# Kernel optimization log

Measured on AMD Instinct MI355X. Metric: run time of the kernel, lower is better.

The kernel has to match this reference:

```python
import jax, jax.numpy as jnp
import numpy as np

EMBED_DIM = 768
HEADS = 8
HEAD_DIM = 128  # gnn_hidden_dim
OUT_DIM = HEADS * HEAD_DIM  # 1024, concat=True
NEG_SLOPE = 0.2  # PyG GATConv leaky_relu slope


def setup_inputs() -> dict:
    key = jax.random.key(0)
    ks = jax.random.split(key, 12)
    N, E = 10000, 160000
    x = jax.random.normal(ks[0], (N, EMBED_DIM), dtype=jnp.float32)
    edge_index = jax.random.randint(ks[1], (2, E), 0, N, dtype=jnp.int32)
    edge_attr = jax.random.uniform(ks[2], (E, 1), dtype=jnp.float32)
    # GATConv params (single layer, edge_dim=1)
    sc = 1.0 / np.sqrt(EMBED_DIM)
    W = jax.random.normal(ks[3], (EMBED_DIM, OUT_DIM), dtype=jnp.float32) * sc
    att_src = jax.random.normal(ks[4], (HEADS, HEAD_DIM), dtype=jnp.float32) * 0.1
    att_dst = jax.random.normal(ks[5], (HEADS, HEAD_DIM), dtype=jnp.float32) * 0.1
    W_edge = jax.random.normal(ks[6], (1, OUT_DIM), dtype=jnp.float32)
    att_edge = jax.random.normal(ks[7], (HEADS, HEAD_DIM), dtype=jnp.float32) * 0.1
    bias = jnp.zeros((OUT_DIM,), dtype=jnp.float32)
    # final classifier: in = 3*OUT_DIM (global pool + text node + image node)
    clf_W = jax.random.normal(ks[8], (3 * OUT_DIM, 2), dtype=jnp.float32) * (1.0 / np.sqrt(3 * OUT_DIM))
    clf_b = jnp.zeros((2,), dtype=jnp.float32)
    return {
        'x': x, 'edge_index': edge_index, 'edge_attr': edge_attr,
        'text_idx': 0, 'image_idx': 1,
        'W': W, 'att_src': att_src, 'att_dst': att_dst,
        'W_edge': W_edge, 'att_edge': att_edge, 'bias': bias,
        'clf_W': clf_W, 'clf_b': clf_b,
    }


def gat_layer(x, edge_index, edge_attr, W, att_src, att_dst, W_edge, att_edge, bias):
    N = x.shape[0]
    # add self-loops with edge_attr = mean of existing edge_attr (PyG default fill_value='mean')
    loop = jnp.arange(N, dtype=edge_index.dtype)
    ei = jnp.concatenate([edge_index, jnp.stack([loop, loop])], axis=1)
    ea_mean = jnp.mean(edge_attr, axis=0, keepdims=True)
    ea = jnp.concatenate([edge_attr, jnp.broadcast_to(ea_mean, (N, edge_attr.shape[1]))], axis=0)
    src, dst = ei[0], ei[1]
    xs = (x @ W).reshape(N, HEADS, HEAD_DIM)             # [N, H, C]
    a_src = jnp.einsum('nhc,hc->nh', xs, att_src)        # per-node src logits
    a_dst = jnp.einsum('nhc,hc->nh', xs, att_dst)
    e_emb = (ea @ W_edge).reshape(-1, HEADS, HEAD_DIM)   # [Etot, H, C]
    a_edge = jnp.einsum('ehc,hc->eh', e_emb, att_edge)
    alpha = jax.nn.leaky_relu(a_src[src] + a_dst[dst] + a_edge, NEG_SLOPE)  # [Etot, H]
    # softmax over incoming edges of each dst node
    m = jax.ops.segment_max(alpha, dst, num_segments=N)
    ex = jnp.exp(alpha - m[dst])
    denom = jax.ops.segment_sum(ex, dst, num_segments=N)
    w = ex / denom[dst]                                  # normalized attention [Etot, H]
    msg = xs[src] * w[:, :, None]                        # [Etot, H, C]
    out = jax.ops.segment_sum(msg, dst, num_segments=N)  # [N, H, C]
    return out.reshape(N, OUT_DIM) + bias


def reference(x, edge_index, edge_attr, text_idx, image_idx,
              W, att_src, att_dst, W_edge, att_edge, bias, clf_W, clf_b):
    # single GAT layer (num_gat_layers=1 -> no ELU/dropout after, eval mode)
    h = gat_layer(x, edge_index, edge_attr, W, att_src, att_dst, W_edge, att_edge, bias)
    g = jnp.mean(h, axis=0, keepdims=True)               # global_mean_pool, batch=None
    t = h[text_idx][None, :]
    im = h[image_idx][None, :]
    fused = jnp.concatenate([g, t, im], axis=1)          # [1, 3*OUT_DIM]
    logits = fused @ clf_W + clf_b                       # [1, 2]
    return logits
```

## Files before the change

kernel.cpp:

```cpp
#include <hip/hip_runtime.h>

#define NN 10000
#define EE 160000
#define ETOT (EE + NN)
#define EMB 768
#define ODIM 1024
#define NEG 0.2f
#define CAP 56

#define OFF_P      0
#define OFF_Q      12288
#define OFF_EAACC  12296
#define OFF_CNTD   12304
#define OFF_CNTS   22304
#define ZERO_START 12296
#define ZERO_CNT   20008
#define OFF_A      32304
#define OFF_SRCD   192304
#define OFF_AED    752304
#define OFF_DSTS   1312304
#define OFF_AES    1872304
#define OFF_RDEN   2432304
#define OFF_Z      2512304
#define OFF_YPART  2524592

#define SELF_MARK 3.0e38f

__global__ __launch_bounds__(256) void k1f(
    const float* __restrict__ W, const float* __restrict__ att_src,
    const float* __restrict__ att_dst, const float* __restrict__ W_edge,
    const float* __restrict__ att_edge, const float* __restrict__ edge_attr,
    const float* __restrict__ bias, const float* __restrict__ clf_W,
    const float* __restrict__ clf_b, float* __restrict__ out,
    const int* __restrict__ ei, float* __restrict__ ws) {
  int b = blockIdx.x;
  if (b < 48) {
    int tid = b * 256 + threadIdx.x;
    int k = tid >> 4, j = tid & 15, h = j & 7;
    const float* att = (j < 8) ? att_src : att_dst;
    const float4* wp = (const float4*)(W + k * ODIM + h * 128);
    const float4* ap = (const float4*)(att + h * 128);
    float acc = 0.f;
    #pragma unroll 8
    for (int c = 0; c < 32; ++c) {
      float4 w4 = wp[c], a4 = ap[c];
      acc += w4.x * a4.x + w4.y * a4.y + w4.z * a4.z + w4.w * a4.w;
    }
    ws[OFF_P + k * 16 + j] = acc;
  } else if (b == 48) {
    if (threadIdx.x < 8) {
      int h = threadIdx.x;
      float acc = 0.f;
      #pragma unroll 8
      for (int c = 0; c < 128; ++c) acc += W_edge[h * 128 + c] * att_edge[h * 128 + c];
      ws[OFF_Q + h] = acc;
    }
  } else if (b == 49) {
    __shared__ float red[8];
    int t = threadIdx.x;
    float b0 = 0.f, b1 = 0.f;
    for (int i = t; i < 3072; i += 256) {
      float f = bias[i & 1023];
      b0 += f * clf_W[2 * i];
      b1 += f * clf_W[2 * i + 1];
    }
    #pragma unroll
    for (int o = 32; o > 0; o >>= 1) {
      b0 += __shfl_down(b0, o, 64);
      b1 += __shfl_down(b1, o, 64);
    }
    if ((t & 63) == 0) { red[(t >> 6) * 2] = b0; red[(t >> 6) * 2 + 1] = b1; }
    __syncthreads();
    if (t == 0) {
      out[0] = clf_b[0] + red[0] + red[2] + red[4] + red[6];
      out[1] = clf_b[1] + red[1] + red[3] + red[5] + red[7];
    }
  } else if (b < 114) {
    int bi = b - 50;
    float acc = 0.f;
    for (int i = bi * 256 + threadIdx.x; i < EE; i += 64 * 256) acc += edge_attr[i];
    #pragma unroll
    for (int off = 32; off > 0; off >>= 1) acc += __shfl_down(acc, off, 64);
    if ((threadIdx.x & 63) == 0) atomicAdd(&ws[OFF_EAACC], acc);
  } else {
    int e = (b - 114) * 256 + threadIdx.x;
    if (e >= ETOT) return;
    int src, dst; float ea;
    if (e < EE) { src = ei[e]; dst = ei[EE + e]; ea = edge_attr[e]; }
    else { src = dst = e - EE; ea = SELF_MARK; }
    int* cntd = (int*)(ws + OFF_CNTD);
    int* cnts = (int*)(ws + OFF_CNTS);
    int pd = atomicAdd(&cntd[dst], 1);
    if (pd < CAP) {
      ((int*)(ws + OFF_SRCD))[dst * CAP + pd] = src;
      ws[OFF_AED + dst * CAP + pd] = ea;
    }
    int ps = atomicAdd(&cnts[src], 1);
    if (ps < CAP) {
      ((int*)(ws + OFF_DSTS))[src * CAP + ps] = dst;
      ws[OFF_AES + src * CAP + ps] = ea;
    }
  }
}

__global__ __launch_bounds__(256) void kAx(const float* __restrict__ x,
                                           float* __restrict__ ws) {
  __shared__ float smem[12288];
  for (int i = threadIdx.x; i < 3072; i += 256)
    ((float4*)smem)[i] = ((const float4*)(ws + OFF_P))[i];
  __syncthreads();
  int nl = threadIdx.x & 31, cg = threadIdx.x >> 5;
  int n = blockIdx.x * 32 + nl;
  float a[16];
  #pragma unroll
  for (int j = 0; j < 16; ++j) a[j] = 0.f;
  if (n < NN) {
    const float4* xr = (const float4*)(x + n * EMB + cg * 96);
    for (int kk = 0; kk < 24; ++kk) {
      float4 xv = xr[kk];
      const float* pr = &smem[(cg * 96 + kk * 4) * 16];
      #pragma unroll
      for (int j = 0; j < 16; ++j) a[j] += xv.x * pr[j];
      #pragma unroll
      for (int j = 0; j < 16; ++j) a[j] += xv.y * pr[16 + j];
      #pragma unroll
      for (int j = 0; j < 16; ++j) a[j] += xv.z * pr[32 + j];
      #pragma unroll
      for (int j = 0; j < 16; ++j) a[j] += xv.w * pr[48 + j];
    }
  }
  __syncthreads();
  #pragma unroll
  for (int j = 0; j < 16; ++j) smem[(cg * 16 + j) * 33 + nl] = a[j];
  __syncthreads();
  for (int w = threadIdx.x; w < 512; w += 256) {
    int rnl = w >> 4, j = w & 15;
    int nn = blockIdx.x * 32 + rnl;
    if (nn < NN) {
      float s = 0.f;
      #pragma unroll
      for (int c2 = 0; c2 < 8; ++c2) s += smem[(c2 * 16 + j) * 33 + rnl];
      ws[OFF_A + nn * 16 + j] = s;
    }
  }
}

__global__ __launch_bounds__(128) void kD(float* __restrict__ ws) {
  int t = blockIdx.x * 128 + threadIdx.x;
  int dst = t >> 3, h = t & 7;
  int deg = ((const int*)(ws + OFF_CNTD))[dst];
  if (deg > CAP) deg = CAP;
  float adh = ws[OFF_A + dst * 16 + 8 + h];
  float qh = ws[OFF_Q + h];
  float mean = ws[OFF_EAACC] * (1.0f / EE);
  const int* srow = (const int*)(ws + OFF_SRCD) + dst * CAP;
  const float* aerow = ws + OFF_AED + dst * CAP;
  float den = 0.f;
  for (int j = 0; j < deg; ++j) {
    float ae = aerow[j];
    if (ae > 1e37f) ae = mean;
    float v = ws[OFF_A + srow[j] * 16 + h] + adh + ae * qh;
    v = (v >= 0.f) ? v : NEG * v;
    den += __expf(v);
  }
  ws[OFF_RDEN + t] = 1.0f / den;
}

__global__ __launch_bounds__(256) void kSYZ(const float* __restrict__ x,
                                            const int* __restrict__ tptr,
                                            const int* __restrict__ iptr,
                                            float* __restrict__ ws) {
  __shared__ float sL[512];
  __shared__ int srcS[CAP];
  float mean = ws[OFF_EAACC] * (1.0f / EE);
  if (blockIdx.x < 471) {
    int bx = blockIdx.x / 3, c = blockIdx.x % 3;
    int base = bx * 64;
    for (int t = threadIdx.x; t < 512; t += 256) {
      int n = base + (t >> 3), h = t & 7;
      float s = 0.f;
      if (n < NN) {
        int deg = ((const int*)(ws + OFF_CNTS))[n];
        if (deg > CAP) deg = CAP;
        float ash = ws[OFF_A + n * 16 + h];
        float qh = ws[OFF_Q + h];
        const int* drow = (const int*)(ws + OFF_DSTS) + n * CAP;
        const float* aerow = ws + OFF_AES + n * CAP;
        for (int j = 0; j < deg; ++j) {
          int dd = drow[j];
          float ae = aerow[j];
          if (ae > 1e37f) ae = mean;
          float v = ash + ws[OFF_A + dd * 16 + 8 + h] + ae * qh;
          v = (v >= 0.f) ? v : NEG * v;
          s += __expf(v) * ws[OFF_RDEN + dd * 8 + h];
        }
      }
      sL[t] = s;
    }
    __syncthreads();
    int col = c * 256 + threadIdx.x;
    float acc[8];
    #pragma unroll
    for (int h = 0; h < 8; ++h) acc[h] = 0.f;
    int nmax = (NN - base < 64) ? (NN - base) : 64;
    for (int i = 0; i < nmax; ++i) {
      float xv = x[(base + i) * EMB + col];
      const float* sv = &sL[i * 8];
      #pragma unroll
      for (int h = 0; h < 8; ++h) acc[h] += xv * sv[h];
    }
    float* yp = ws + OFF_YPART + bx * 6144 + col;
    #pragma unroll
    for (int h = 0; h < 8; ++h) yp[h * 768] = acc[h];
  } else {
    int r = blockIdx.x - 471;
    int d = r / 3, kc = r % 3;
    int target = (d == 0) ? tptr[0] : iptr[0];
    int deg = ((const int*)(ws + OFF_CNTD))[target];
    if (deg > CAP) deg = CAP;
    for (int idx = threadIdx.x; idx < deg * 8; idx += 256) {
      int j = idx >> 3, h = idx & 7;
      int srcj = ((const int*)(ws + OFF_SRCD))[target * CAP + j];
      float ae = ws[OFF_AED + target * CAP + j];
      if (ae > 1e37f) ae = mean;
      float v = ws[OFF_A + srcj * 16 + h] + ws[OFF_A + target * 16 + 8 + h]
              + ae * ws[OFF_Q + h];
      v = (v >= 0.f) ? v : NEG * v;
      sL[idx] = __expf(v) * ws[OFF_RDEN + target * 8 + h];
      if (h == 0) srcS[j] = srcj;
    }
    __syncthreads();
    int col = kc * 256 + threadIdx.x;
    float acc[8];
    #pragma unroll
    for (int h = 0; h < 8; ++h) acc[h] = 0.f;
    for (int j = 0; j < deg; ++j) {
      float xv = x[srcS[j] * EMB + col];
      const float* wv = &sL[j * 8];
      #pragma unroll
      for (int h = 0; h < 8; ++h) acc[h] += wv[h] * xv;
    }
    #pragma unroll
    for (int h = 0; h < 8; ++h) ws[OFF_Z + (d * 8 + h) * EMB + col] = acc[h];
  }
}

__global__ __launch_bounds__(128) void k8(const float* __restrict__ W,
                                          const float* __restrict__ clf_W,
                                          float* __restrict__ out,
                                          float* __restrict__ ws) {
  __shared__ float vL[144];
  __shared__ float red[4];
  int h = blockIdx.x, kc = blockIdx.y, kbase = kc * 48;
  for (int i = threadIdx.x; i < 144; i += 128) {
    int d = i / 48, k = i - d * 48;
    float v;
    if (d == 0) {
      float acc = 0.f;
      for (int b = 0; b < 157; ++b)
        acc += ws[OFF_YPART + b * 6144 + h * 768 + kbase + k];
      v = acc * (1.0f / NN);
    } else {
      v = ws[OFF_Z + ((d - 1) * 8 + h) * 768 + kbase + k];
    }
    vL[i] = v;
  }
  __syncthreads();
  int c = threadIdx.x;
  float a0 = 0.f, a1 = 0.f, a2 = 0.f;
  #pragma unroll 4
  for (int k = 0; k < 48; ++k) {
    float wv = W[(kbase + k) * ODIM + h * 128 + c];
    a0 += vL[k] * wv;
    a1 += vL[48 + k] * wv;
    a2 += vL[96 + k] * wv;
  }
  int ib = h * 128 + c;
  float l0 = a0 * clf_W[2 * ib] + a1 * clf_W[2 * (1024 + ib)]
           + a2 * clf_W[2 * (2048 + ib)];
  float l1 = a0 * clf_W[2 * ib + 1] + a1 * clf_W[2 * (1024 + ib) + 1]
           + a2 * clf_W[2 * (2048 + ib) + 1];
  #pragma unroll
  for (int o = 32; o > 0; o >>= 1) {
    l0 += __shfl_down(l0, o, 64);
    l1 += __shfl_down(l1, o, 64);
  }
  if ((threadIdx.x & 63) == 0) {
    red[(threadIdx.x >> 6) * 2] = l0;
    red[(threadIdx.x >> 6) * 2 + 1] = l1;
  }
  __syncthreads();
  if (threadIdx.x == 0) {
    atomicAdd(&out[0], red[0] + red[2]);
    atomicAdd(&out[1], red[1] + red[3]);
  }
}

extern "C" void kernel_launch(void* const* d_in, const int* in_sizes, int n_in,
                              void* d_out, int out_size, void* d_ws, size_t ws_size,
                              hipStream_t stream) {
  const float* x        = (const float*)d_in[0];
  const int*   ei       = (const int*)d_in[1];
  const float* edge_attr= (const float*)d_in[2];
  const int*   tptr     = (const int*)d_in[3];
  const int*   iptr     = (const int*)d_in[4];
  const float* W        = (const float*)d_in[5];
  const float* att_src  = (const float*)d_in[6];
  const float* att_dst  = (const float*)d_in[7];
  const float* W_edge   = (const float*)d_in[8];
  const float* att_edge = (const float*)d_in[9];
  const float* bias     = (const float*)d_in[10];
  const float* clf_W    = (const float*)d_in[11];
  const float* clf_b    = (const float*)d_in[12];
  float* ws  = (float*)d_ws;
  float* out = (float*)d_out;

  hipMemsetAsync(ws + ZERO_START, 0, ZERO_CNT * sizeof(float), stream);
  k1f<<<779, 256, 0, stream>>>(W, att_src, att_dst, W_edge, att_edge, edge_attr,
                               bias, clf_W, clf_b, out, ei, ws);
  kAx<<<313, 256, 0, stream>>>(x, ws);
  kD<<<625, 128, 0, stream>>>(ws);
  kSYZ<<<477, 256, 0, stream>>>(x, tptr, iptr, ws);
  dim3 g8(8, 16);
  k8<<<g8, 128, 0, stream>>>(W, clf_W, out, ws);
}
```

Measured before the change: 192.8 us.

## Merge memset and five kernels into one cooperative persistent kernel with grid syncs

```diff
diff --git a/kernel.cpp b/kernel.cpp
--- a/kernel.cpp
+++ b/kernel.cpp
@@ -1,4 +1,7 @@
 #include <hip/hip_runtime.h>
+#include <hip/hip_cooperative_groups.h>
+
+namespace cg = cooperative_groups;
 
 #define NN 10000
 #define EE 160000
@@ -25,17 +28,26 @@
 #define OFF_YPART  2524592
 
 #define SELF_MARK 3.0e38f
-
-__global__ __launch_bounds__(256) void k1f(
-    const float* __restrict__ W, const float* __restrict__ att_src,
-    const float* __restrict__ att_dst, const float* __restrict__ W_edge,
-    const float* __restrict__ att_edge, const float* __restrict__ edge_attr,
+#define GRID 512
+#define GSZ (GRID * 256)
+
+__global__ __launch_bounds__(256, 2) void mega(
+    const float* __restrict__ x, const int* __restrict__ ei,
+    const float* __restrict__ edge_attr, const int* __restrict__ tptr,
+    const int* __restrict__ iptr, const float* __restrict__ W,
+    const float* __restrict__ att_src, const float* __restrict__ att_dst,
+    const float* __restrict__ W_edge, const float* __restrict__ att_edge,
     const float* __restrict__ bias, const float* __restrict__ clf_W,
     const float* __restrict__ clf_b, float* __restrict__ out,
-    const int* __restrict__ ei, float* __restrict__ ws) {
-  int b = blockIdx.x;
-  if (b < 48) {
-    int tid = b * 256 + threadIdx.x;
+    float* __restrict__ ws) {
+  cg::grid_group grid = cg::this_grid();
+  __shared__ float smem[12288];
+  const int gtid = blockIdx.x * 256 + threadIdx.x;
+
+  for (int i = gtid; i < ZERO_CNT; i += GSZ) ws[ZERO_START + i] = 0.f;
+  grid.sync();
+
+  for (int tid = gtid; tid < 12288; tid += GSZ) {
     int k = tid >> 4, j = tid & 15, h = j & 7;
     const float* att = (j < 8) ? att_src : att_dst;
     const float4* wp = (const float4*)(W + k * ODIM + h * 128);
@@ -46,17 +58,17 @@
       float4 w4 = wp[c], a4 = ap[c];
       acc += w4.x * a4.x + w4.y * a4.y + w4.z * a4.z + w4.w * a4.w;
     }
-    ws[OFF_P + k * 16 + j] = acc;
-  } else if (b == 48) {
-    if (threadIdx.x < 8) {
-      int h = threadIdx.x;
-      float acc = 0.f;
-      #pragma unroll 8
-      for (int c = 0; c < 128; ++c) acc += W_edge[h * 128 + c] * att_edge[h * 128 + c];
-      ws[OFF_Q + h] = acc;
-    }
-  } else if (b == 49) {
-    __shared__ float red[8];
+    ws[OFF_P + tid] = acc;
+  }
+  if (gtid < 8) {
+    int h = gtid;
+    float acc = 0.f;
+    #pragma unroll 8
+    for (int c = 0; c < 128; ++c) acc += W_edge[h * 128 + c] * att_edge[h * 128 + c];
+    ws[OFF_Q + h] = acc;
+  }
+  if (blockIdx.x == 1) {
+    float* red = smem;
     int t = threadIdx.x;
     float b0 = 0.f, b1 = 0.f;
     for (int i = t; i < 3072; i += 256) {
@@ -75,16 +87,16 @@
       out[0] = clf_b[0] + red[0] + red[2] + red[4] + red[6];
       out[1] = clf_b[1] + red[1] + red[3] + red[5] + red[7];
     }
-  } else if (b < 114) {
-    int bi = b - 50;
+  }
+  if (blockIdx.x >= 64 && blockIdx.x < 128) {
     float acc = 0.f;
-    for (int i = bi * 256 + threadIdx.x; i < EE; i += 64 * 256) acc += edge_attr[i];
+    for (int i = (blockIdx.x - 64) * 256 + threadIdx.x; i < EE; i += 64 * 256)
+      acc += edge_attr[i];
     #pragma unroll
-    for (int off = 32; off > 0; off >>= 1) acc += __shfl_down(acc, off, 64);
+    for (int o = 32; o > 0; o >>= 1) acc += __shfl_down(acc, o, 64);
     if ((threadIdx.x & 63) == 0) atomicAdd(&ws[OFF_EAACC], acc);
-  } else {
-    int e = (b - 114) * 256 + threadIdx.x;
-    if (e >= ETOT) return;
+  }
+  for (int e = gtid; e < ETOT; e += GSZ) {
     int src, dst; float ea;
     if (e < EE) { src = ei[e]; dst = ei[EE + e]; ea = edge_attr[e]; }
     else { src = dst = e - EE; ea = SELF_MARK; }
@@ -101,198 +113,199 @@
       ws[OFF_AES + src * CAP + ps] = ea;
     }
   }
-}
-
-__global__ __launch_bounds__(256) void kAx(const float* __restrict__ x,
-                                           float* __restrict__ ws) {
-  __shared__ float smem[12288];
-  for (int i = threadIdx.x; i < 3072; i += 256)
-    ((float4*)smem)[i] = ((const float4*)(ws + OFF_P))[i];
-  __syncthreads();
-  int nl = threadIdx.x & 31, cg = threadIdx.x >> 5;
-  int n = blockIdx.x * 32 + nl;
-  float a[16];
-  #pragma unroll
-  for (int j = 0; j < 16; ++j) a[j] = 0.f;
-  if (n < NN) {
-    const float4* xr = (const float4*)(x + n * EMB + cg * 96);
-    for (int kk = 0; kk < 24; ++kk) {
-      float4 xv = xr[kk];
-      const float* pr = &smem[(cg * 96 + kk * 4) * 16];
+  grid.sync();
+
+  {
+    for (int i = threadIdx.x; i < 3072; i += 256)
+      ((float4*)smem)[i] = ((const float4*)(ws + OFF_P))[i];
+    __syncthreads();
+    for (int tile = blockIdx.x; tile < 313; tile += GRID) {
+      int nl = threadIdx.x & 31, cgp = threadIdx.x >> 5;
+      int n = tile * 32 + nl;
+      float a[16];
       #pragma unroll
-      for (int j = 0; j < 16; ++j) a[j] += xv.x * pr[j];
+      for (int j = 0; j < 16; ++j) a[j] = 0.f;
+      if (n < NN) {
+        const float4* xr = (const float4*)(x + n * EMB + cgp * 96);
+        for (int kk = 0; kk < 24; ++kk) {
+          float4 xv = xr[kk];
+          const float* pr = &smem[(cgp * 96 + kk * 4) * 16];
+          #pragma unroll
+          for (int j = 0; j < 16; ++j) a[j] += xv.x * pr[j];
+          #pragma unroll
+          for (int j = 0; j < 16; ++j) a[j] += xv.y * pr[16 + j];
+          #pragma unroll
+          for (int j = 0; j < 16; ++j) a[j] += xv.z * pr[32 + j];
+          #pragma unroll
+          for (int j = 0; j < 16; ++j) a[j] += xv.w * pr[48 + j];
+        }
+      }
+      __syncthreads();
       #pragma unroll
-      for (int j = 0; j < 16; ++j) a[j] += xv.y * pr[16 + j];
-      #pragma unroll
-      for (int j = 0; j < 16; ++j) a[j] += xv.z * pr[32 + j];
-      #pragma unroll
-      for (int j = 0; j < 16; ++j) a[j] += xv.w * pr[48 + j];
-    }
-  }
-  __syncthreads();
-  #pragma unroll
-  for (int j = 0; j < 16; ++j) smem[(cg * 16 + j) * 33 + nl] = a[j];
-  __syncthreads();
-  for (int w = threadIdx.x; w < 512; w += 256) {
-    int rnl = w >> 4, j = w & 15;
-    int nn = blockIdx.x * 32 + rnl;
-    if (nn < NN) {
-      float s = 0.f;
-      #pragma unroll
-      for (int c2 = 0; c2 < 8; ++c2) s += smem[(c2 * 16 + j) * 33 + rnl];
-      ws[OFF_A + nn * 16 + j] = s;
-    }
-  }
-}
-
-__global__ __launch_bounds__(128) void kD(float* __restrict__ ws) {
-  int t = blockIdx.x * 128 + threadIdx.x;
-  int dst = t >> 3, h = t & 7;
-  int deg = ((const int*)(ws + OFF_CNTD))[dst];
-  if (deg > CAP) deg = CAP;
-  float adh = ws[OFF_A + dst * 16 + 8 + h];
-  float qh = ws[OFF_Q + h];
-  float mean = ws[OFF_EAACC] * (1.0f / EE);
-  const int* srow = (const int*)(ws + OFF_SRCD) + dst * CAP;
-  const float* aerow = ws + OFF_AED + dst * CAP;
-  float den = 0.f;
-  for (int j = 0; j < deg; ++j) {
-    float ae = aerow[j];
-    if (ae > 1e37f) ae = mean;
-    float v = ws[OFF_A + srow[j] * 16 + h] + adh + ae * qh;
-    v = (v >= 0.f) ? v : NEG * v;
-    den += __expf(v);
-  }
-  ws[OFF_RDEN + t] = 1.0f / den;
-}
-
-__global__ __launch_bounds__(256) void kSYZ(const float* __restrict__ x,
-                                            const int* __restrict__ tptr,
-                                            const int* __restrict__ iptr,
-                                            float* __restrict__ ws) {
-  __shared__ float sL[512];
-  __shared__ int srcS[CAP];
-  float mean = ws[OFF_EAACC] * (1.0f / EE);
-  if (blockIdx.x < 471) {
-    int bx = blockIdx.x / 3, c = blockIdx.x % 3;
-    int base = bx * 64;
-    for (int t = threadIdx.x; t < 512; t += 256) {
-      int n = base + (t >> 3), h = t & 7;
-      float s = 0.f;
-      if (n < NN) {
-        int deg = ((const int*)(ws + OFF_CNTS))[n];
+      for (int j = 0; j < 16; ++j) smem[(cgp * 16 + j) * 33 + nl] = a[j];
+      __syncthreads();
+      for (int w = threadIdx.x; w < 512; w += 256) {
+        int rnl = w >> 4, j = w & 15;
+        int nn = tile * 32 + rnl;
+        if (nn < NN) {
+          float s = 0.f;
+          #pragma unroll
+          for (int c2 = 0; c2 < 8; ++c2) s += smem[(c2 * 16 + j) * 33 + rnl];
+          ws[OFF_A + nn * 16 + j] = s;
+        }
+      }
+    }
+  }
+  grid.sync();
+
+  for (int t = gtid; t < 80000; t += GSZ) {
+    int dst = t >> 3, h = t & 7;
+    int deg = ((const int*)(ws + OFF_CNTD))[dst];
+    if (deg > CAP) deg = CAP;
+    float adh = ws[OFF_A + dst * 16 + 8 + h];
+    float qh = ws[OFF_Q + h];
+    float mean = ws[OFF_EAACC] * (1.0f / EE);
+    const int* srow = (const int*)(ws + OFF_SRCD) + dst * CAP;
+    const float* aerow = ws + OFF_AED + dst * CAP;
+    float den = 0.f;
+    for (int j = 0; j < deg; ++j) {
+      float ae = aerow[j];
+      if (ae > 1e37f) ae = mean;
+      float v = ws[OFF_A + srow[j] * 16 + h] + adh + ae * qh;
+      v = (v >= 0.f) ? v : NEG * v;
+      den += __expf(v);
+    }
+    ws[OFF_RDEN + t] = 1.0f / den;
+  }
+  grid.sync();
+
+  {
+    float* sL = smem;
+    int* srcS = (int*)(smem + 512);
+    for (int task = blockIdx.x; task < 477; task += GRID) {
+      float mean = ws[OFF_EAACC] * (1.0f / EE);
+      if (task < 471) {
+        int bx = task / 3, c = task % 3;
+        int base = bx * 64;
+        for (int t = threadIdx.x; t < 512; t += 256) {
+          int n = base + (t >> 3), h = t & 7;
+          float s = 0.f;
+          if (n < NN) {
+            int deg = ((const int*)(ws + OFF_CNTS))[n];
+            if (deg > CAP) deg = CAP;
+            float ash = ws[OFF_A + n * 16 + h];
+            float qh = ws[OFF_Q + h];
+            const int* drow = (const int*)(ws + OFF_DSTS) + n * CAP;
+            const float* aerow = ws + OFF_AES + n * CAP;
+            for (int j = 0; j < deg; ++j) {
+              int dd = drow[j];
+              float ae = aerow[j];
+              if (ae > 1e37f) ae = mean;
+              float v = ash + ws[OFF_A + dd * 16 + 8 + h] + ae * qh;
+              v = (v >= 0.f) ? v : NEG * v;
+              s += __expf(v) * ws[OFF_RDEN + dd * 8 + h];
+            }
+          }
+          sL[t] = s;
+        }
+        __syncthreads();
+        int col = c * 256 + threadIdx.x;
+        float acc[8];
+        #pragma unroll
+        for (int h = 0; h < 8; ++h) acc[h] = 0.f;
+        int nmax = (NN - base < 64) ? (NN - base) : 64;
+        for (int i = 0; i < nmax; ++i) {
+          float xv = x[(base + i) * EMB + col];
+          const float* sv = &sL[i * 8];
+          #pragma unroll
+          for (int h = 0; h < 8; ++h) acc[h] += xv * sv[h];
+        }
+        float* yp = ws + OFF_YPART + bx * 6144 + col;
+        #pragma unroll
+        for (int h = 0; h < 8; ++h) yp[h * 768] = acc[h];
+      } else {
+        int r = task - 471;
+        int d = r / 3, kc = r % 3;
+        int target = (d == 0) ? tptr[0] : iptr[0];
+        int deg = ((const int*)(ws + OFF_CNTD))[target];
         if (deg > CAP) deg = CAP;
-        float ash = ws[OFF_A + n * 16 + h];
-        float qh = ws[OFF_Q + h];
-        const int* drow = (const int*)(ws + OFF_DSTS) + n * CAP;
-        const float* aerow = ws + OFF_AES + n * CAP;
+        for (int idx = threadIdx.x; idx < deg * 8; idx += 256) {
+          int j = idx >> 3, h = idx & 7;
+          int srcj = ((const int*)(ws + OFF_SRCD))[target * CAP + j];
+          float ae = ws[OFF_AED + target * CAP + j];
+          if (ae > 1e37f) ae = mean;
+          float v = ws[OFF_A + srcj * 16 + h] + ws[OFF_A + target * 16 + 8 + h]
+                  + ae * ws[OFF_Q + h];
+          v = (v >= 0.f) ? v : NEG * v;
+          sL[idx] = __expf(v) * ws[OFF_RDEN + target * 8 + h];
+          if (h == 0) srcS[j] = srcj;
+        }
+        __syncthreads();
+        int col = kc * 256 + threadIdx.x;
+        float acc[8];
+        #pragma unroll
+        for (int h = 0; h < 8; ++h) acc[h] = 0.f;
         for (int j = 0; j < deg; ++j) {
-          int dd = drow[j];
-          float ae = aerow[j];
-          if (ae > 1e37f) ae = mean;
-          float v = ash + ws[OFF_A + dd * 16 + 8 + h] + ae * qh;
-          v = (v >= 0.f) ? v : NEG * v;
-          s += __expf(v) * ws[OFF_RDEN + dd * 8 + h];
-        }
+          float xv = x[srcS[j] * EMB + col];
+          const float* wv = &sL[j * 8];
+          #pragma unroll
+          for (int h = 0; h < 8; ++h) acc[h] += wv[h] * xv;
+        }
+        #pragma unroll
+        for (int h = 0; h < 8; ++h) ws[OFF_Z + (d * 8 + h) * EMB + col] = acc[h];
       }
-      sL[t] = s;
+    }
+  }
+  grid.sync();
+
+  if (blockIdx.x < 64) {
+    int half = threadIdx.x >> 7;
+    int task = blockIdx.x * 2 + half;
+    int h = task >> 4, kc = task & 15, kbase = kc * 48;
+    int c = threadIdx.x & 127;
+    float* vL = smem + half * 256;
+    float* red = smem + 512 + half * 4;
+    for (int i = c; i < 144; i += 128) {
+      int d = i / 48, k = i - d * 48;
+      float v;
+      if (d == 0) {
+        float acc = 0.f;
+        for (int b = 0; b < 157; ++b)
+          acc += ws[OFF_YPART + b * 6144 + h * 768 + kbase + k];
+        v = acc * (1.0f / NN);
+      } else {
+        v = ws[OFF_Z + ((d - 1) * 8 + h) * 768 + kbase + k];
+      }
+      vL[i] = v;
     }
     __syncthreads();
-    int col = c * 256 + threadIdx.x;
-    float acc[8];
+    float a0 = 0.f, a1 = 0.f, a2 = 0.f;
+    #pragma unroll 4
+    for (int k = 0; k < 48; ++k) {
+      float wv = W[(kbase + k) * ODIM + h * 128 + c];
+      a0 += vL[k] * wv;
+      a1 += vL[48 + k] * wv;
+      a2 += vL[96 + k] * wv;
+    }
+    int ib = h * 128 + c;
+    float l0 = a0 * clf_W[2 * ib] + a1 * clf_W[2 * (1024 + ib)]
+             + a2 * clf_W[2 * (2048 + ib)];
+    float l1 = a0 * clf_W[2 * ib + 1] + a1 * clf_W[2 * (1024 + ib) + 1]
+             + a2 * clf_W[2 * (2048 + ib) + 1];
     #pragma unroll
-    for (int h = 0; h < 8; ++h) acc[h] = 0.f;
-    int nmax = (NN - base < 64) ? (NN - base) : 64;
-    for (int i = 0; i < nmax; ++i) {
-      float xv = x[(base + i) * EMB + col];
-      const float* sv = &sL[i * 8];
-      #pragma unroll
-      for (int h = 0; h < 8; ++h) acc[h] += xv * sv[h];
-    }
-    float* yp = ws + OFF_YPART + bx * 6144 + col;
-    #pragma unroll
-    for (int h = 0; h < 8; ++h) yp[h * 768] = acc[h];
-  } else {
-    int r = blockIdx.x - 471;
-    int d = r / 3, kc = r % 3;
-    int target = (d == 0) ? tptr[0] : iptr[0];
-    int deg = ((const int*)(ws + OFF_CNTD))[target];
-    if (deg > CAP) deg = CAP;
-    for (int idx = threadIdx.x; idx < deg * 8; idx += 256) {
-      int j = idx >> 3, h = idx & 7;
-      int srcj = ((const int*)(ws + OFF_SRCD))[target * CAP + j];
-      float ae = ws[OFF_AED + target * CAP + j];
-      if (ae > 1e37f) ae = mean;
-      float v = ws[OFF_A + srcj * 16 + h] + ws[OFF_A + target * 16 + 8 + h]
-              + ae * ws[OFF_Q + h];
-      v = (v >= 0.f) ? v : NEG * v;
-      sL[idx] = __expf(v) * ws[OFF_RDEN + target * 8 + h];
-      if (h == 0) srcS[j] = srcj;
+    for (int o = 32; o > 0; o >>= 1) {
+      l0 += __shfl_down(l0, o, 64);
+      l1 += __shfl_down(l1, o, 64);
+    }
+    if ((threadIdx.x & 63) == 0) {
+      red[((threadIdx.x >> 6) & 1) * 2] = l0;
+      red[((threadIdx.x >> 6) & 1) * 2 + 1] = l1;
     }
     __syncthreads();
-    int col = kc * 256 + threadIdx.x;
-    float acc[8];
-    #pragma unroll
-    for (int h = 0; h < 8; ++h) acc[h] = 0.f;
-    for (int j = 0; j < deg; ++j) {
-      float xv = x[srcS[j] * EMB + col];
-      const float* wv = &sL[j * 8];
-      #pragma unroll
-      for (int h = 0; h < 8; ++h) acc[h] += wv[h] * xv;
-    }
-    #pragma unroll
-    for (int h = 0; h < 8; ++h) ws[OFF_Z + (d * 8 + h) * EMB + col] = acc[h];
-  }
-}
-
-__global__ __launch_bounds__(128) void k8(const float* __restrict__ W,
-                                          const float* __restrict__ clf_W,
-                                          float* __restrict__ out,
-                                          float* __restrict__ ws) {
-  __shared__ float vL[144];
-  __shared__ float red[4];
-  int h = blockIdx.x, kc = blockIdx.y, kbase = kc * 48;
-  for (int i = threadIdx.x; i < 144; i += 128) {
-    int d = i / 48, k = i - d * 48;
-    float v;
-    if (d == 0) {
-      float acc = 0.f;
-      for (int b = 0; b < 157; ++b)
-        acc += ws[OFF_YPART + b * 6144 + h * 768 + kbase + k];
-      v = acc * (1.0f / NN);
-    } else {
-      v = ws[OFF_Z + ((d - 1) * 8 + h) * 768 + kbase + k];
-    }
-    vL[i] = v;
-  }
-  __syncthreads();
-  int c = threadIdx.x;
-  float a0 = 0.f, a1 = 0.f, a2 = 0.f;
-  #pragma unroll 4
-  for (int k = 0; k < 48; ++k) {
-    float wv = W[(kbase + k) * ODIM + h * 128 + c];
-    a0 += vL[k] * wv;
-    a1 += vL[48 + k] * wv;
-    a2 += vL[96 + k] * wv;
-  }
-  int ib = h * 128 + c;
-  float l0 = a0 * clf_W[2 * ib] + a1 * clf_W[2 * (1024 + ib)]
-           + a2 * clf_W[2 * (2048 + ib)];
-  float l1 = a0 * clf_W[2 * ib + 1] + a1 * clf_W[2 * (1024 + ib) + 1]
-           + a2 * clf_W[2 * (2048 + ib) + 1];
-  #pragma unroll
-  for (int o = 32; o > 0; o >>= 1) {
-    l0 += __shfl_down(l0, o, 64);
-    l1 += __shfl_down(l1, o, 64);
-  }
-  if ((threadIdx.x & 63) == 0) {
-    red[(threadIdx.x >> 6) * 2] = l0;
-    red[(threadIdx.x >> 6) * 2 + 1] = l1;
-  }
-  __syncthreads();
-  if (threadIdx.x == 0) {
-    atomicAdd(&out[0], red[0] + red[2]);
-    atomicAdd(&out[1], red[1] + red[3]);
+    if (c == 0) {
+      atomicAdd(&out[0], red[0] + red[2]);
+      atomicAdd(&out[1], red[1] + red[3]);
+    }
   }
 }
 
@@ -315,12 +328,9 @@
   float* ws  = (float*)d_ws;
   float* out = (float*)d_out;
 
-  hipMemsetAsync(ws + ZERO_START, 0, ZERO_CNT * sizeof(float), stream);
-  k1f<<<779, 256, 0, stream>>>(W, att_src, att_dst, W_edge, att_edge, edge_attr,
-                               bias, clf_W, clf_b, out, ei, ws);
-  kAx<<<313, 256, 0, stream>>>(x, ws);
-  kD<<<625, 128, 0, stream>>>(ws);
-  kSYZ<<<477, 256, 0, stream>>>(x, tptr, iptr, ws);
-  dim3 g8(8, 16);
-  k8<<<g8, 128, 0, stream>>>(W, clf_W, out, ws);
+  void* args[] = {
+    (void*)&x, (void*)&ei, (void*)&edge_attr, (void*)&tptr, (void*)&iptr,
+    (void*)&W, (void*)&att_src, (void*)&att_dst, (void*)&W_edge, (void*)&att_edge,
+    (void*)&bias, (void*)&clf_W, (void*)&clf_b, (void*)&out, (void*)&ws };
+  hipLaunchCooperativeKernel((void*)mega, dim3(GRID), dim3(256), args, 0, stream);
 }
```

After: 497.6 us. 2.58x slower.

## Fold classifier weights into W and fuse aggregation with final reduction

Applied to the files above, without the earlier changes.

```diff
diff --git a/kernel.cpp b/kernel.cpp
--- a/kernel.cpp
+++ b/kernel.cpp
@@ -21,8 +21,7 @@
 #define OFF_DSTS   1312304
 #define OFF_AES    1872304
 #define OFF_RDEN   2432304
-#define OFF_Z      2512304
-#define OFF_YPART  2524592
+#define OFF_G      2512304
 
 #define SELF_MARK 3.0e38f
 
@@ -46,7 +45,7 @@
       float4 w4 = wp[c], a4 = ap[c];
       acc += w4.x * a4.x + w4.y * a4.y + w4.z * a4.z + w4.w * a4.w;
     }
-    ws[OFF_P + k * 16 + j] = acc;
+    ws[OFF_P + tid] = acc;
   } else if (b == 48) {
     if (threadIdx.x < 8) {
       int h = threadIdx.x;
@@ -75,15 +74,35 @@
       out[0] = clf_b[0] + red[0] + red[2] + red[4] + red[6];
       out[1] = clf_b[1] + red[1] + red[3] + red[5] + red[7];
     }
-  } else if (b < 114) {
-    int bi = b - 50;
+  } else if (b < 74) {
+    int t = (b - 50) * 256 + threadIdx.x;
+    int k = t >> 3, h = t & 7;
+    const float4* wseg = (const float4*)(W + k * ODIM + h * 128);
+    float acc[6] = {0.f, 0.f, 0.f, 0.f, 0.f, 0.f};
+    for (int c4 = 0; c4 < 32; ++c4) {
+      float4 wv = wseg[c4];
+      #pragma unroll
+      for (int d = 0; d < 3; ++d) {
+        const float4* cp = (const float4*)(clf_W + 2 * (1024 * d + h * 128 + c4 * 4));
+        float4 q0 = cp[0], q1 = cp[1];
+        acc[d * 2 + 0] += wv.x * q0.x + wv.y * q0.z + wv.z * q1.x + wv.w * q1.z;
+        acc[d * 2 + 1] += wv.x * q0.y + wv.y * q0.w + wv.z * q1.y + wv.w * q1.w;
+      }
+    }
+    #pragma unroll
+    for (int d = 0; d < 3; ++d) {
+      ws[OFF_G + d * 12288 + k * 16 + h * 2 + 0] = acc[d * 2 + 0];
+      ws[OFF_G + d * 12288 + k * 16 + h * 2 + 1] = acc[d * 2 + 1];
+    }
+  } else if (b < 138) {
+    int bi = b - 74;
     float acc = 0.f;
     for (int i = bi * 256 + threadIdx.x; i < EE; i += 64 * 256) acc += edge_attr[i];
     #pragma unroll
     for (int off = 32; off > 0; off >>= 1) acc += __shfl_down(acc, off, 64);
     if ((threadIdx.x & 63) == 0) atomicAdd(&ws[OFF_EAACC], acc);
   } else {
-    int e = (b - 114) * 256 + threadIdx.x;
+    int e = (b - 138) * 256 + threadIdx.x;
     if (e >= ETOT) return;
     int src, dst; float ea;
     if (e < EE) { src = ei[e]; dst = ei[EE + e]; ea = edge_attr[e]; }
@@ -156,6 +175,7 @@
   const int* srow = (const int*)(ws + OFF_SRCD) + dst * CAP;
   const float* aerow = ws + OFF_AED + dst * CAP;
   float den = 0.f;
+  #pragma unroll 4
   for (int j = 0; j < deg; ++j) {
     float ae = aerow[j];
     if (ae > 1e37f) ae = mean;
@@ -166,59 +186,77 @@
   ws[OFF_RDEN + t] = 1.0f / den;
 }
 
-__global__ __launch_bounds__(256) void kSYZ(const float* __restrict__ x,
-                                            const int* __restrict__ tptr,
-                                            const int* __restrict__ iptr,
-                                            float* __restrict__ ws) {
-  __shared__ float sL[512];
-  __shared__ int srcS[CAP];
+__global__ __launch_bounds__(256, 3) void kF(const float* __restrict__ x,
+                                             const int* __restrict__ tptr,
+                                             const int* __restrict__ iptr,
+                                             float* __restrict__ out,
+                                             float* __restrict__ ws) {
+  __shared__ float smem[12864];
+  int t = threadIdx.x;
   float mean = ws[OFF_EAACC] * (1.0f / EE);
-  if (blockIdx.x < 471) {
-    int bx = blockIdx.x / 3, c = blockIdx.x % 3;
-    int base = bx * 64;
-    for (int t = threadIdx.x; t < 512; t += 256) {
-      int n = base + (t >> 3), h = t & 7;
+  float c0 = 0.f, c1 = 0.f;
+  float scale;
+  if (blockIdx.x < 625) {
+    scale = 1.0f / NN;
+    int base = blockIdx.x * 16;
+    if (t >= 128) {
+      for (int i = t - 128; i < 3072; i += 128)
+        ((float4*)smem)[i] = ((const float4*)(ws + OFF_G))[i];
+    } else {
+      int nl = t >> 3, h = t & 7;
+      int n = base + nl;
+      int deg = ((const int*)(ws + OFF_CNTS))[n];
+      if (deg > CAP) deg = CAP;
+      float ash = ws[OFF_A + n * 16 + h];
+      float qh = ws[OFF_Q + h];
+      const int* drow = (const int*)(ws + OFF_DSTS) + n * CAP;
+      const float* aerow = ws + OFF_AES + n * CAP;
       float s = 0.f;
-      if (n < NN) {
-        int deg = ((const int*)(ws + OFF_CNTS))[n];
-        if (deg > CAP) deg = CAP;
-        float ash = ws[OFF_A + n * 16 + h];
-        float qh = ws[OFF_Q + h];
-        const int* drow = (const int*)(ws + OFF_DSTS) + n * CAP;
-        const float* aerow = ws + OFF_AES + n * CAP;
-        for (int j = 0; j < deg; ++j) {
-          int dd = drow[j];
-          float ae = aerow[j];
-          if (ae > 1e37f) ae = mean;
-          float v = ash + ws[OFF_A + dd * 16 + 8 + h] + ae * qh;
-          v = (v >= 0.f) ? v : NEG * v;
-          s += __expf(v) * ws[OFF_RDEN + dd * 8 + h];
-        }
+      #pragma unroll 4
+      for (int j = 0; j < deg; ++j) {
+        int dd = drow[j];
+        float ae = aerow[j];
+        if (ae > 1e37f) ae = mean;
+        float v = ash + ws[OFF_A + dd * 16 + 8 + h] + ae * qh;
+        v = (v >= 0.f) ? v : NEG * v;
+        s += __expf(v) * ws[OFF_RDEN + dd * 8 + h];
       }
-      sL[t] = s;
+      smem[12288 + nl * 8 + h] = s;
     }
     __syncthreads();
-    int col = c * 256 + threadIdx.x;
-    float acc[8];
-    #pragma unroll
-    for (int h = 0; h < 8; ++h) acc[h] = 0.f;
-    int nmax = (NN - base < 64) ? (NN - base) : 64;
-    for (int i = 0; i < nmax; ++i) {
-      float xv = x[(base + i) * EMB + col];
-      const float* sv = &sL[i * 8];
-      #pragma unroll
-      for (int h = 0; h < 8; ++h) acc[h] += xv * sv[h];
-    }
-    float* yp = ws + OFF_YPART + bx * 6144 + col;
-    #pragma unroll
-    for (int h = 0; h < 8; ++h) yp[h * 768] = acc[h];
+    int nl = t & 15, cgp = t >> 4;
+    int n = base + nl;
+    float a[16];
+    #pragma unroll
+    for (int j = 0; j < 16; ++j) a[j] = 0.f;
+    const float4* xr = (const float4*)(x + n * EMB + cgp * 48);
+    for (int kk = 0; kk < 12; ++kk) {
+      float4 xv = xr[kk];
+      const float* pr = &smem[(cgp * 48 + kk * 4) * 16];
+      #pragma unroll
+      for (int j = 0; j < 16; ++j) a[j] += xv.x * pr[j];
+      #pragma unroll
+      for (int j = 0; j < 16; ++j) a[j] += xv.y * pr[16 + j];
+      #pragma unroll
+      for (int j = 0; j < 16; ++j) a[j] += xv.z * pr[32 + j];
+      #pragma unroll
+      for (int j = 0; j < 16; ++j) a[j] += xv.w * pr[48 + j];
+    }
+    #pragma unroll
+    for (int h = 0; h < 8; ++h) {
+      float sv = smem[12288 + nl * 8 + h];
+      c0 += sv * a[2 * h];
+      c1 += sv * a[2 * h + 1];
+    }
   } else {
-    int r = blockIdx.x - 471;
-    int d = r / 3, kc = r % 3;
+    scale = 1.0f;
+    int d = blockIdx.x - 625;
     int target = (d == 0) ? tptr[0] : iptr[0];
+    for (int i = t; i < 3072; i += 256)
+      ((float4*)smem)[i] = ((const float4*)(ws + OFF_G + (d + 1) * 12288))[i];
     int deg = ((const int*)(ws + OFF_CNTD))[target];
     if (deg > CAP) deg = CAP;
-    for (int idx = threadIdx.x; idx < deg * 8; idx += 256) {
+    for (int idx = t; idx < deg * 8; idx += 256) {
       int j = idx >> 3, h = idx & 7;
       int srcj = ((const int*)(ws + OFF_SRCD))[target * CAP + j];
       float ae = ws[OFF_AED + target * CAP + j];
@@ -226,73 +264,55 @@
       float v = ws[OFF_A + srcj * 16 + h] + ws[OFF_A + target * 16 + 8 + h]
               + ae * ws[OFF_Q + h];
       v = (v >= 0.f) ? v : NEG * v;
-      sL[idx] = __expf(v) * ws[OFF_RDEN + target * 8 + h];
-      if (h == 0) srcS[j] = srcj;
+      smem[12288 + j * 8 + h] = __expf(v) * ws[OFF_RDEN + target * 8 + h];
+      if (h == 0) ((int*)smem)[12800 + j] = srcj;
     }
     __syncthreads();
-    int col = kc * 256 + threadIdx.x;
-    float acc[8];
-    #pragma unroll
-    for (int h = 0; h < 8; ++h) acc[h] = 0.f;
-    for (int j = 0; j < deg; ++j) {
-      float xv = x[srcS[j] * EMB + col];
-      const float* wv = &sL[j * 8];
-      #pragma unroll
-      for (int h = 0; h < 8; ++h) acc[h] += wv[h] * xv;
-    }
-    #pragma unroll
-    for (int h = 0; h < 8; ++h) ws[OFF_Z + (d * 8 + h) * EMB + col] = acc[h];
-  }
-}
-
-__global__ __launch_bounds__(128) void k8(const float* __restrict__ W,
-                                          const float* __restrict__ clf_W,
-                                          float* __restrict__ out,
-                                          float* __restrict__ ws) {
-  __shared__ float vL[144];
-  __shared__ float red[4];
-  int h = blockIdx.x, kc = blockIdx.y, kbase = kc * 48;
-  for (int i = threadIdx.x; i < 144; i += 128) {
-    int d = i / 48, k = i - d * 48;
-    float v;
-    if (d == 0) {
-      float acc = 0.f;
-      for (int b = 0; b < 157; ++b)
-        acc += ws[OFF_YPART + b * 6144 + h * 768 + kbase + k];
-      v = acc * (1.0f / NN);
-    } else {
-      v = ws[OFF_Z + ((d - 1) * 8 + h) * 768 + kbase + k];
-    }
-    vL[i] = v;
-  }
-  __syncthreads();
-  int c = threadIdx.x;
-  float a0 = 0.f, a1 = 0.f, a2 = 0.f;
-  #pragma unroll 4
-  for (int k = 0; k < 48; ++k) {
-    float wv = W[(kbase + k) * ODIM + h * 128 + c];
-    a0 += vL[k] * wv;
-    a1 += vL[48 + k] * wv;
-    a2 += vL[96 + k] * wv;
-  }
-  int ib = h * 128 + c;
-  float l0 = a0 * clf_W[2 * ib] + a1 * clf_W[2 * (1024 + ib)]
-           + a2 * clf_W[2 * (2048 + ib)];
-  float l1 = a0 * clf_W[2 * ib + 1] + a1 * clf_W[2 * (1024 + ib) + 1]
-           + a2 * clf_W[2 * (2048 + ib) + 1];
+    int nl = t & 15, cgp = t >> 4;
+    for (int jb = 0; jb * 16 < deg; ++jb) {
+      int j = jb * 16 + nl;
+      int n = (j < deg) ? ((int*)smem)[12800 + j] : 0;
+      float a[16];
+      #pragma unroll
+      for (int jj = 0; jj < 16; ++jj) a[jj] = 0.f;
+      const float4* xr = (const float4*)(x + n * EMB + cgp * 48);
+      for (int kk = 0; kk < 12; ++kk) {
+        float4 xv = xr[kk];
+        const float* pr = &smem[(cgp * 48 + kk * 4) * 16];
+        #pragma unroll
+        for (int jj = 0; jj < 16; ++jj) a[jj] += xv.x * pr[jj];
+        #pragma unroll
+        for (int jj = 0; jj < 16; ++jj) a[jj] += xv.y * pr[16 + jj];
+        #pragma unroll
+        for (int jj = 0; jj < 16; ++jj) a[jj] += xv.z * pr[32 + jj];
+        #pragma unroll
+        for (int jj = 0; jj < 16; ++jj) a[jj] += xv.w * pr[48 + jj];
+      }
+      if (j < deg) {
+        #pragma unroll
+        for (int h = 0; h < 8; ++h) {
+          float wv = smem[12288 + j * 8 + h];
+          c0 += wv * a[2 * h];
+          c1 += wv * a[2 * h + 1];
+        }
+      }
+    }
+  }
   #pragma unroll
   for (int o = 32; o > 0; o >>= 1) {
-    l0 += __shfl_down(l0, o, 64);
-    l1 += __shfl_down(l1, o, 64);
-  }
-  if ((threadIdx.x & 63) == 0) {
-    red[(threadIdx.x >> 6) * 2] = l0;
-    red[(threadIdx.x >> 6) * 2 + 1] = l1;
+    c0 += __shfl_down(c0, o, 64);
+    c1 += __shfl_down(c1, o, 64);
+  }
+  if ((t & 63) == 0) {
+    smem[12856 + (t >> 6) * 2] = c0;
+    smem[12857 + (t >> 6) * 2] = c1;
   }
   __syncthreads();
-  if (threadIdx.x == 0) {
-    atomicAdd(&out[0], red[0] + red[2]);
-    atomicAdd(&out[1], red[1] + red[3]);
+  if (t == 0) {
+    float r0 = smem[12856] + smem[12858] + smem[12860] + smem[12862];
+    float r1 = smem[12857] + smem[12859] + smem[12861] + smem[12863];
+    atomicAdd(&out[0], r0 * scale);
+    atomicAdd(&out[1], r1 * scale);
   }
 }
 
@@ -316,11 +336,9 @@
   float* out = (float*)d_out;
 
   hipMemsetAsync(ws + ZERO_START, 0, ZERO_CNT * sizeof(float), stream);
-  k1f<<<779, 256, 0, stream>>>(W, att_src, att_dst, W_edge, att_edge, edge_attr,
+  k1f<<<803, 256, 0, stream>>>(W, att_src, att_dst, W_edge, att_edge, edge_attr,
                                bias, clf_W, clf_b, out, ei, ws);
   kAx<<<313, 256, 0, stream>>>(x, ws);
   kD<<<625, 128, 0, stream>>>(ws);
-  kSYZ<<<477, 256, 0, stream>>>(x, tptr, iptr, ws);
-  dim3 g8(8, 16);
-  k8<<<g8, 128, 0, stream>>>(W, clf_W, out, ws);
-}
+  kF<<<627, 256, 0, stream>>>(x, tptr, iptr, out, ws);
+}
```

Measured after the change: 186.2 us. -3.4%, faster.
